# Optimization experiments

Measured on AMD Instinct MI355X. Metric: run time of the kernel, lower is better.

## Reference

```python
import jax, jax.numpy as jnp
import numpy as np

THETA = 10000.0
H, D_NOPE, D_ROPE, D_V = 12, 64, 64, 128
D_MODEL, D_LAT = 768, 128
B, S = 4, 2048


def _rope(x, pos, theta=THETA):
    # x: (B, S, D) with D even; pos: (S,) int. Matches RoPE.forward exactly
    # (interleaved even/odd rotation, freqs over full flattened D).
    D = x.shape[-1]
    inv_freq = 1.0 / theta ** (jnp.arange(0, D, 2, dtype=jnp.float32) / D)
    ang = pos.astype(jnp.float32)[:, None] * inv_freq        # (S, D/2)
    c, s = jnp.cos(ang), jnp.sin(ang)
    xe, xo = x[..., 0::2], x[..., 1::2]
    out = jnp.stack([xe * c - xo * s, xe * s + xo * c], axis=-1)
    return out.reshape(x.shape)


def setup_inputs() -> dict:
    key = jax.random.key(0)
    ks = jax.random.split(key, 12)
    std = 0.02
    inp = {
        'x': jax.random.normal(ks[0], (B, S, D_MODEL), jnp.float32),
        'token_positions': jnp.arange(S, dtype=jnp.int64) if jax.config.jax_enable_x64 else jnp.arange(S, dtype=jnp.int32),
        'W_dkv': jax.random.normal(ks[1], (D_LAT, D_MODEL), jnp.float32) * std,
        'b_dkv': jnp.zeros((D_LAT,), jnp.float32),
        'W_dq': jax.random.normal(ks[2], (D_LAT, D_MODEL), jnp.float32) * std,
        'b_dq': jnp.zeros((D_LAT,), jnp.float32),
        'W_uk_nope': jax.random.normal(ks[3], (H * D_NOPE, D_LAT), jnp.float32) * std,
        'b_uk_nope': jnp.zeros((H * D_NOPE,), jnp.float32),
        'W_uv': jax.random.normal(ks[4], (H * D_V, D_LAT), jnp.float32) * std,
        'b_uv': jnp.zeros((H * D_V,), jnp.float32),
        'W_uq_nope': jax.random.normal(ks[5], (H * D_NOPE, D_LAT), jnp.float32) * std,
        'b_uq_nope': jnp.zeros((H * D_NOPE,), jnp.float32),
        'W_uq_rope': jax.random.normal(ks[6], (H * D_ROPE, D_LAT), jnp.float32) * std,
        'b_uq_rope': jnp.zeros((H * D_ROPE,), jnp.float32),
        'W_uk_rope': jax.random.normal(ks[7], (H * D_ROPE, D_MODEL), jnp.float32) * std,
        'b_uk_rope': jnp.zeros((H * D_ROPE,), jnp.float32),
        'W_o': jax.random.normal(ks[8], (D_MODEL, H * D_V), jnp.float32) * std,
        'b_o': jnp.zeros((D_MODEL,), jnp.float32),
    }
    return inp


def reference(x, token_positions, W_dkv, b_dkv, W_dq, b_dq,
              W_uk_nope, b_uk_nope, W_uv, b_uv, W_uq_nope, b_uq_nope,
              W_uq_rope, b_uq_rope, W_uk_rope, b_uk_rope, W_o, b_o):
    b, s, _ = x.shape
    lin = lambda t, W, bb: t @ W.T + bb
    d_qk = D_NOPE + D_ROPE  # 128

    C_kv = lin(x, W_dkv, b_dkv)               # (B,S,128)
    C_q = lin(x, W_dq, b_dq)                  # (B,S,128)

    q_nope = lin(C_q, W_uq_nope, b_uq_nope)   # (B,S,H*64)
    k_nope = lin(C_kv, W_uk_nope, b_uk_nope)  # (B,S,H*64)
    v = lin(C_kv, W_uv, b_uv)                 # (B,S,H*128)

    q_rope = _rope(lin(C_q, W_uq_rope, b_uq_rope), token_positions)
    k_rope = _rope(lin(x, W_uk_rope, b_uk_rope), token_positions)

    # Faithful to torch: concat flattened nope||rope then view into heads.
    q = jnp.concatenate([q_nope, q_rope], axis=-1).reshape(b, s, H, d_qk).transpose(0, 2, 1, 3)
    k = jnp.concatenate([k_nope, k_rope], axis=-1).reshape(b, s, H, d_qk).transpose(0, 2, 1, 3)
    vh = v.reshape(b, s, H, D_V).transpose(0, 2, 1, 3)

    scale = 1.0 / jnp.sqrt(jnp.asarray(d_qk, x.dtype))
    logits = jnp.einsum('bhqd,bhkd->bhqk', q, k) * scale
    causal = jnp.tril(jnp.ones((s, s), bool))
    logits = jnp.where(causal, logits, jnp.finfo(logits.dtype).min)
    attn = jax.nn.softmax(logits, axis=-1)
    o = jnp.einsum('bhqk,bhkd->bhqd', attn, vh)      # (B,H,S,Dv)
    o = o.transpose(0, 2, 1, 3).reshape(b, s, H * D_V)
    return o @ W_o.T + b_o
```

## Files before the change

### kernel.cpp

```cpp
#include <hip/hip_runtime.h>

typedef __attribute__((ext_vector_type(8))) short short8;
typedef __attribute__((ext_vector_type(4))) short short4v;
typedef __attribute__((ext_vector_type(2))) int int2v;
typedef __attribute__((ext_vector_type(4))) float float4v;

#define MFMA16(a, b, c) __builtin_amdgcn_mfma_f32_16x16x32_bf16((a), (b), (c), 0, 0, 0)

__device__ __forceinline__ short f2bf(float f) {
  unsigned u = __float_as_uint(f);
  u += 0x7fffu + ((u >> 16) & 1u);
  return (short)(u >> 16);
}

__device__ __forceinline__ int cvtpk(float a, float b) {
  int r;
  asm("v_cvt_pk_bf16_f32 %0, %1, %2" : "=v"(r) : "v"(a), "v"(b));
  return r;
}

__device__ __forceinline__ void glds16(const short* g, short* l) {
  __builtin_amdgcn_global_load_lds(
      (const __attribute__((address_space(1))) void*)g,
      (__attribute__((address_space(3))) void*)l, 16, 0, 0);
}

struct CastSeg { const float* src; short* dst; int n4; };
struct CastArgs { CastSeg seg[9]; int start[10]; };

__global__ __launch_bounds__(256) void castk(CastArgs a) {
  int blk = blockIdx.x;
  int si = 0;
#pragma unroll
  for (int i = 1; i < 9; i++) si += (blk >= a.start[i]);
  int i = (blk - a.start[si]) * 256 + threadIdx.x;
  if (i >= a.seg[si].n4) return;
  float4v f = ((const float4v*)a.seg[si].src)[i];
  short4v o;
  o[0] = f2bf(f[0]); o[1] = f2bf(f[1]); o[2] = f2bf(f[2]); o[3] = f2bf(f[3]);
  ((short4v*)a.seg[si].dst)[i] = o;
}

struct GSeg {
  const short* A;
  const short* W;
  const float* bias0;
  const float* bias1;
  void* outp;
  int lda, ldw, bsplit, ropestart, ldo, ocol, K, flags;
};
struct GArgs { GSeg s[3]; int start[4]; };

__global__ __launch_bounds__(256, 2) void gemm_rt(GArgs ga, const int* __restrict__ pos) {
  int bx = blockIdx.x;
  int si = (bx >= ga.start[1]) + (bx >= ga.start[2]);
  const GSeg sg = ga.s[si];
  int tid = threadIdx.x, w = tid >> 6, lane = tid & 63;
  int quad = lane >> 4, l16 = lane & 15;
  int bm = blockIdx.y * 128, bn = (bx - ga.start[si]) * 128;
  int wm = (w & 1) * 64, wn = (w >> 1) * 64;
  int lda = sg.lda, ldw = sg.ldw;

  __shared__ short At[2][128 * 64];
  __shared__ short Bt[2][128 * 64];

  int srow[4], soff[4];
#pragma unroll
  for (int j = 0; j < 4; j++) {
    int r = w * 32 + j * 8 + (lane >> 3);
    srow[j] = r;
    soff[j] = ((lane & 7) ^ (r & 7)) << 3;
  }
  const short* Ag = sg.A + (size_t)bm * lda;
  const short* Wg = sg.W + (size_t)bn * ldw;

  float4v acc[4][4];
  float4v z = {0.f, 0.f, 0.f, 0.f};
#pragma unroll
  for (int mi = 0; mi < 4; mi++)
#pragma unroll
    for (int ni = 0; ni < 4; ni++) acc[mi][ni] = z;

  auto comp = [&](const short* Ab, const short* Bb) {
#pragma unroll
    for (int ks = 0; ks < 2; ks++) {
      short8 af[4], bf[4];
#pragma unroll
      for (int mi = 0; mi < 4; mi++) {
        int row = wm + mi * 16 + l16;
        af[mi] = *(const short8*)&Ab[(row << 6) + ((((ks << 2) + quad) ^ (row & 7)) << 3)];
      }
#pragma unroll
      for (int ni = 0; ni < 4; ni++) {
        int row = wn + ni * 16 + l16;
        bf[ni] = *(const short8*)&Bb[(row << 6) + ((((ks << 2) + quad) ^ (row & 7)) << 3)];
      }
#pragma unroll
      for (int mi = 0; mi < 4; mi++)
#pragma unroll
        for (int ni = 0; ni < 4; ni++)
          acc[mi][ni] = MFMA16(af[mi], bf[ni], acc[mi][ni]);
    }
  };

  int nk = sg.K >> 6;
  if (nk == 2) {
#pragma unroll
    for (int j = 0; j < 4; j++) {
      glds16(Ag + (size_t)srow[j] * lda + soff[j], &At[0][(w * 32 + j * 8) * 64]);
      glds16(Ag + (size_t)srow[j] * lda + 64 + soff[j], &At[1][(w * 32 + j * 8) * 64]);
      glds16(Wg + (size_t)srow[j] * ldw + soff[j], &Bt[0][(w * 32 + j * 8) * 64]);
      glds16(Wg + (size_t)srow[j] * ldw + 64 + soff[j], &Bt[1][(w * 32 + j * 8) * 64]);
    }
    __syncthreads();
    comp(At[0], Bt[0]);
    comp(At[1], Bt[1]);
  } else {
#pragma unroll
    for (int j = 0; j < 4; j++)
      glds16(Ag + (size_t)srow[j] * lda + soff[j], &At[0][(w * 32 + j * 8) * 64]);
#pragma unroll
    for (int j = 0; j < 4; j++)
      glds16(Wg + (size_t)srow[j] * ldw + soff[j], &Bt[0][(w * 32 + j * 8) * 64]);
    for (int it = 0; it < nk; it++) {
      __syncthreads();
      if (it + 1 < nk) {
        int kt = (it + 1) << 6, nb = (it + 1) & 1;
#pragma unroll
        for (int j = 0; j < 4; j++)
          glds16(Ag + (size_t)srow[j] * lda + kt + soff[j],
                 &At[nb][(w * 32 + j * 8) * 64]);
#pragma unroll
        for (int j = 0; j < 4; j++)
          glds16(Wg + (size_t)srow[j] * ldw + kt + soff[j],
                 &Bt[nb][(w * 32 + j * 8) * 64]);
      }
      comp(At[it & 1], Bt[it & 1]);
    }
  }

  bool ropeF = sg.flags & 1, scaleF = sg.flags & 2;
  bool vtF = sg.flags & 4, f32F = sg.flags & 8;
#pragma unroll
  for (int ni = 0; ni < 4; ni++) {
    int col = bn + wn + ni * 16 + l16;
    float bv = (col < sg.bsplit) ? sg.bias0[col] : sg.bias1[col - sg.bsplit];
    float fr = 0.f;
    bool dorope = ropeF && (col >= sg.ropestart);
    if (dorope) {
      int ri = (col - sg.ropestart) & ~1;
      fr = exp2f((float)ri * (-13.287712379549449f / 768.0f));
    }
#pragma unroll
    for (int mi = 0; mi < 4; mi++) {
      int row0 = bm + wm + mi * 16 + quad * 4;
      if (vtF) {
        int bidx = row0 >> 11, s = row0 & 2047;
        short4v ov;
#pragma unroll
        for (int r = 0; r < 4; r++) ov[r] = f2bf(acc[mi][ni][r] + bv);
        *(short4v*)((short*)sg.outp + ((size_t)(bidx * 1536 + col)) * 2048 + s) = ov;
      } else {
#pragma unroll
        for (int r = 0; r < 4; r++) {
          int row = row0 + r;
          float v = acc[mi][ni][r] + bv;
          if (ropeF) {
            float pv = __shfl_xor(v, 1, 64);
            if (dorope) {
              float ang = (float)pos[row & 2047] * fr;
              float sn, cs;
              __sincosf(ang, &sn, &cs);
              v = (col & 1) ? (pv * sn + v * cs) : (v * cs - pv * sn);
            }
          }
          if (scaleF) v *= 0.12751743f;
          if (f32F)
            ((float*)sg.outp)[(size_t)row * sg.ldo + sg.ocol + col] = v;
          else
            ((short*)sg.outp)[(size_t)row * sg.ldo + sg.ocol + col] = f2bf(v);
        }
      }
    }
  }
}

__global__ __launch_bounds__(256, 2) void mla_attn(const short* __restrict__ Q,
                                                   const short* __restrict__ K,
                                                   const short* __restrict__ Vt,
                                                   short* __restrict__ O) {
  const int ld = 1536, SEQ = 2048;
  int tid = threadIdx.x, w = tid >> 6, lane = tid & 63;
  int quad = lane >> 4, l16 = lane & 15;
  int o = (int)blockIdx.x;
  int rank = o / 48;
  int g = o - rank * 48;
  int qt = (15 - rank) * 128;
  int hh = g % 12, b = g / 12;
  int qw = qt + w * 32;

  __shared__ short Kt[2][64 * 128];
  __shared__ short Vl[2][128 * 64];
  __shared__ short Pm[4][32 * 64];
  char* pwB = (char*)Pm[w];

  int kgo[4], vgo[4];
#pragma unroll
  for (int j = 0; j < 4; j++) {
    int rk = (w * 4 + j) * 4 + (lane >> 4);
    kgo[j] = rk * ld + (((lane & 15) ^ (rk & 7)) << 3);
    int rv = (w * 4 + j) * 8 + (lane >> 3);
    vgo[j] = rv * SEQ + (((lane & 7) ^ (rv & 7)) << 3);
  }
  const short* Kg = K + (size_t)b * SEQ * ld + hh * 128;
  const short* Vg = Vt + (size_t)(b * 12 + hh) * 128 * SEQ;

  short8 qf[2][4];
  {
    const short* Qg = Q + (size_t)(b * SEQ + qw + l16) * ld + hh * 128 + quad * 8;
#pragma unroll
    for (int nf = 0; nf < 2; nf++)
#pragma unroll
      for (int ks = 0; ks < 4; ks++)
        qf[nf][ks] = *(const short8*)(Qg + (size_t)nf * 16 * ld + ks * 32);
  }

  int koff[4][4], voff[2][8], pfo[2][2], pwo[2][4];
#pragma unroll
  for (int ks = 0; ks < 4; ks++)
#pragma unroll
    for (int mf = 0; mf < 4; mf++) {
      int row = mf * 16 + l16;
      koff[ks][mf] = row * 256 + ((((ks << 2) + quad) ^ (row & 7)) << 4);
    }
#pragma unroll
  for (int t = 0; t < 2; t++) {
#pragma unroll
    for (int df = 0; df < 8; df++) {
      int vr = df * 16 + l16;
      voff[t][df] = vr * 128 + ((((t << 2) + quad) ^ (vr & 7)) << 4);
    }
#pragma unroll
    for (int mq = 0; mq < 2; mq++)
      pfo[t][mq] = (mq * 16 + l16) * 128 + ((((t << 2) + quad) ^ (l16 & 7)) << 4);
#pragma unroll
    for (int mf = 0; mf < 4; mf++) {
      int p = (mf * 2 + (quad >> 1)) ^ (l16 & 7);
      pwo[t][mf] = (t * 16 + l16) * 128 + (p << 4) + ((quad & 1) << 3);
    }
  }

  float4v z = {0.f, 0.f, 0.f, 0.f};
  float4v oacc[2][8];
#pragma unroll
  for (int mq = 0; mq < 2; mq++)
#pragma unroll
    for (int df = 0; df < 8; df++) oacc[mq][df] = z;
  float l_i[2] = {0.f, 0.f};

#pragma unroll
  for (int j = 0; j < 4; j++) glds16(Kg + kgo[j], &Kt[0][(w * 4 + j) * 512]);
#pragma unroll
  for (int j = 0; j < 4; j++) glds16(Vg + vgo[j], &Vl[0][(w * 4 + j) * 512]);

  int ntiles = (qt >> 6) + 2;

#define ATTN_TILE(IT, NB, NB1)                                                 \
  do {                                                                         \
    int kt = (IT) << 6;                                                        \
    __syncthreads();                                                           \
    if ((IT) + 1 < ntiles) {                                                   \
      const short* kn = Kg + (size_t)(kt + 64) * ld;                           \
      const short* vn = Vg + (kt + 64);                                        \
      _Pragma("unroll") for (int j = 0; j < 4; j++)                            \
          glds16(kn + kgo[j], &Kt[NB1][(w * 4 + j) * 512]);                    \
      _Pragma("unroll") for (int j = 0; j < 4; j++)                            \
          glds16(vn + vgo[j], &Vl[NB1][(w * 4 + j) * 512]);                    \
    }                                                                          \
    if (kt <= qw + 31) {                                                       \
      const char* Kb = (const char*)Kt[NB];                                    \
      const char* Vb = (const char*)Vl[NB];                                    \
      float4v sf[4][2];                                                        \
      __builtin_amdgcn_s_setprio(1);                                           \
      _Pragma("unroll") for (int mf = 0; mf < 4; mf++) {                       \
        short8 a = *(const short8*)(Kb + koff[0][mf]);                         \
        sf[mf][0] = MFMA16(a, qf[0][0], z);                                    \
        sf[mf][1] = MFMA16(a, qf[1][0], z);                                    \
      }                                                                        \
      _Pragma("unroll") for (int ks = 1; ks < 4; ks++) {                       \
        _Pragma("unroll") for (int mf = 0; mf < 4; mf++) {                     \
          short8 a = *(const short8*)(Kb + koff[ks][mf]);                      \
          sf[mf][0] = MFMA16(a, qf[0][ks], sf[mf][0]);                         \
          sf[mf][1] = MFMA16(a, qf[1][ks], sf[mf][1]);                         \
        }                                                                      \
      }                                                                        \
      __builtin_amdgcn_s_setprio(0);                                           \
      if (kt + 63 > qw) {                                                      \
        _Pragma("unroll") for (int mf = 0; mf < 4; mf++) {                     \
          int key = kt + mf * 16 + quad * 4;                                   \
          _Pragma("unroll") for (int nf = 0; nf < 2; nf++) {                   \
            int q = qw + nf * 16 + l16;                                        \
            _Pragma("unroll") for (int r = 0; r < 4; r++)                      \
                if (key + r > q) sf[mf][nf][r] = -3e38f;                       \
          }                                                                    \
        }                                                                      \
      }                                                                        \
      _Pragma("unroll") for (int nf = 0; nf < 2; nf++) {                       \
        float ps = 0.f;                                                        \
        _Pragma("unroll") for (int mf = 0; mf < 4; mf++)                       \
            _Pragma("unroll") for (int r = 0; r < 4; r++) {                    \
          float e = exp2f(sf[mf][nf][r]);                                      \
          sf[mf][nf][r] = e;                                                   \
          ps += e;                                                             \
        }                                                                      \
        l_i[nf] += ps;                                                         \
        _Pragma("unroll") for (int mf = 0; mf < 4; mf++) {                     \
          int2v pk;                                                            \
          pk[0] = cvtpk(sf[mf][nf][0], sf[mf][nf][1]);                         \
          pk[1] = cvtpk(sf[mf][nf][2], sf[mf][nf][3]);                         \
          *(int2v*)(pwB + pwo[nf][mf]) = pk;                                   \
        }                                                                      \
      }                                                                        \
      __builtin_amdgcn_s_setprio(1);                                           \
      _Pragma("unroll") for (int t = 0; t < 2; t++) {                          \
        short8 pf0 = *(const short8*)(pwB + pfo[t][0]);                        \
        short8 pf1 = *(const short8*)(pwB + pfo[t][1]);                        \
        _Pragma("unroll") for (int df = 0; df < 8; df++) {                     \
          short8 vf = *(const short8*)(Vb + voff[t][df]);                      \
          oacc[0][df] = MFMA16(pf0, vf, oacc[0][df]);                          \
          oacc[1][df] = MFMA16(pf1, vf, oacc[1][df]);                          \
        }                                                                      \
      }                                                                        \
      __builtin_amdgcn_s_setprio(0);                                           \
    }                                                                          \
  } while (0)

  for (int it = 0; it < ntiles; it += 2) {
    ATTN_TILE(it, 0, 1);
    ATTN_TILE(it + 1, 1, 0);
  }
#undef ATTN_TILE

  short* Og = O + (size_t)(b * SEQ + qw) * ld + hh * 128;
#pragma unroll
  for (int mq = 0; mq < 2; mq++) {
    float l = l_i[mq];
    l += __shfl_xor(l, 16, 64);
    l += __shfl_xor(l, 32, 64);
    float linv = 1.0f / l;
    float lb[4];
#pragma unroll
    for (int r = 0; r < 4; r++) lb[r] = __shfl(linv, (quad << 2) + r, 64);
#pragma unroll
    for (int df = 0; df < 8; df++)
#pragma unroll
      for (int r = 0; r < 4; r++)
        Og[(size_t)(mq * 16 + (quad << 2) + r) * ld + df * 16 + l16] =
            f2bf(oacc[mq][df][r] * lb[r]);
  }
}

extern "C" void kernel_launch(void* const* d_in, const int* in_sizes, int n_in,
                              void* d_out, int out_size, void* d_ws, size_t ws_size,
                              hipStream_t stream) {
  const int S = 2048, DM = 768, DL = 128, HD = 1536;
  const int M = 4 * S;
  const int BIG = 1 << 28;

  const float* x = (const float*)d_in[0];
  const int* pos = (const int*)d_in[1];
  const float* W_dkv = (const float*)d_in[2];
  const float* b_dkv = (const float*)d_in[3];
  const float* W_dq = (const float*)d_in[4];
  const float* b_dq = (const float*)d_in[5];
  const float* W_uk_nope = (const float*)d_in[6];
  const float* b_uk_nope = (const float*)d_in[7];
  const float* W_uv = (const float*)d_in[8];
  const float* b_uv = (const float*)d_in[9];
  const float* W_uq_nope = (const float*)d_in[10];
  const float* b_uq_nope = (const float*)d_in[11];
  const float* W_uq_rope = (const float*)d_in[12];
  const float* b_uq_rope = (const float*)d_in[13];
  const float* W_uk_rope = (const float*)d_in[14];
  const float* b_uk_rope = (const float*)d_in[15];
  const float* W_o = (const float*)d_in[16];
  const float* b_o = (const float*)d_in[17];

  char* p = (char*)d_ws;
  size_t off = 0;
  auto take = [&](size_t nelem) -> short* {
    short* r = (short*)(p + off);
    off += (nelem * 2 + 255) & ~(size_t)255;
    return r;
  };
  short* xb = take((size_t)M * DM);
  short* Wdq = take(DL * DM);
  short* Wdkv = take(DL * DM);
  short* Wuqnope = take(768 * DL);
  short* Wuqrope = take(768 * DL);
  short* Wuknope = take(768 * DL);
  short* Wuv = take(1536 * DL);
  short* Wukrope = take(768 * DM);
  short* Wo = take(768 * 1536);
  short* Cm = take((size_t)M * 256);
  short* Qm = take((size_t)M * HD);
  short* Km = take((size_t)M * HD);
  short* Vtm = take((size_t)M * HD);
  short* Om = take((size_t)M * HD);
  if (off > ws_size) return;

  CastArgs ca;
  const float* srcs[9] = {x, W_dq, W_dkv, W_uq_nope, W_uq_rope, W_uk_nope, W_uv, W_uk_rope, W_o};
  short* dsts[9] = {xb, Wdq, Wdkv, Wuqnope, Wuqrope, Wuknope, Wuv, Wukrope, Wo};
  int ns[9] = {M * DM, DL * DM, DL * DM, 768 * DL, 768 * DL, 768 * DL, 1536 * DL, 768 * DM, 768 * 1536};
  ca.start[0] = 0;
  for (int i = 0; i < 9; i++) {
    ca.seg[i].src = srcs[i];
    ca.seg[i].dst = dsts[i];
    ca.seg[i].n4 = ns[i] / 4;
    ca.start[i + 1] = ca.start[i] + (ca.seg[i].n4 + 255) / 256;
  }
  castk<<<dim3(ca.start[9]), dim3(256), 0, stream>>>(ca);

  GArgs g1;
  g1.s[0].A = xb;   g1.s[0].W = Wdq;      g1.s[0].bias0 = b_dq;      g1.s[0].bias1 = b_dkv;
  g1.s[0].outp = Cm; g1.s[0].lda = DM; g1.s[0].ldw = DM; g1.s[0].bsplit = 128;
  g1.s[0].ropestart = 0; g1.s[0].ldo = 256; g1.s[0].ocol = 0; g1.s[0].K = DM; g1.s[0].flags = 0;
  g1.s[1].A = xb;   g1.s[1].W = Wukrope;  g1.s[1].bias0 = b_uk_rope; g1.s[1].bias1 = b_uk_rope;
  g1.s[1].outp = Km; g1.s[1].lda = DM; g1.s[1].ldw = DM; g1.s[1].bsplit = BIG;
  g1.s[1].ropestart = 0; g1.s[1].ldo = HD; g1.s[1].ocol = 768; g1.s[1].K = DM; g1.s[1].flags = 1;
  g1.s[2] = g1.s[1];
  g1.start[0] = 0; g1.start[1] = 2; g1.start[2] = 8; g1.start[3] = 8;
  gemm_rt<<<dim3(8, M / 128), dim3(256), 0, stream>>>(g1, pos);

  GArgs g2;
  g2.s[0].A = Cm;   g2.s[0].W = Wuqnope;  g2.s[0].bias0 = b_uq_nope; g2.s[0].bias1 = b_uq_rope;
  g2.s[0].outp = Qm; g2.s[0].lda = 256; g2.s[0].ldw = DL; g2.s[0].bsplit = 768;
  g2.s[0].ropestart = 768; g2.s[0].ldo = HD; g2.s[0].ocol = 0; g2.s[0].K = DL; g2.s[0].flags = 1 | 2;
  g2.s[1].A = Cm + 128; g2.s[1].W = Wuknope; g2.s[1].bias0 = b_uk_nope; g2.s[1].bias1 = b_uk_nope;
  g2.s[1].outp = Km; g2.s[1].lda = 256; g2.s[1].ldw = DL; g2.s[1].bsplit = BIG;
  g2.s[1].ropestart = 0; g2.s[1].ldo = HD; g2.s[1].ocol = 0; g2.s[1].K = DL; g2.s[1].flags = 0;
  g2.s[2].A = Cm + 128; g2.s[2].W = Wuv;   g2.s[2].bias0 = b_uv;      g2.s[2].bias1 = b_uv;
  g2.s[2].outp = Vtm; g2.s[2].lda = 256; g2.s[2].ldw = DL; g2.s[2].bsplit = BIG;
  g2.s[2].ropestart = 0; g2.s[2].ldo = 0; g2.s[2].ocol = 0; g2.s[2].K = DL; g2.s[2].flags = 4;
  g2.start[0] = 0; g2.start[1] = 12; g2.start[2] = 18; g2.start[3] = 30;
  gemm_rt<<<dim3(30, M / 128), dim3(256), 0, stream>>>(g2, pos);

  mla_attn<<<dim3(768), dim3(256), 0, stream>>>(Qm, Km, Vtm, Om);

  GArgs g3;
  g3.s[0].A = Om;   g3.s[0].W = Wo;       g3.s[0].bias0 = b_o;       g3.s[0].bias1 = b_o;
  g3.s[0].outp = d_out; g3.s[0].lda = HD; g3.s[0].ldw = HD; g3.s[0].bsplit = BIG;
  g3.s[0].ropestart = 0; g3.s[0].ldo = 768; g3.s[0].ocol = 0; g3.s[0].K = HD; g3.s[0].flags = 8;
  g3.s[1] = g3.s[0];
  g3.s[2] = g3.s[0];
  g3.start[0] = 0; g3.start[1] = 6; g3.start[2] = 6; g3.start[3] = 6;
  gemm_rt<<<dim3(6, M / 128), dim3(256), 0, stream>>>(g3, pos);
}
```

Before: 311.0 us.

## Reuse A tile across paired N tiles and stage V-transpose stores via LDS

For the K=128 up-projection GEMMs, a block now loads its A tile once and computes two 128-wide N tiles in sequence (pairF flag). The second W tile is staged while the first epilogue runs, so A global traffic and the block count drop. The V-transposed output is now staged through shared memory with a rotated layout and written as coalesced 16-byte rows instead of scattered 8-byte stores. The grid is transposed so M tiles lie along x, which changes block scheduling order. The cost is fewer blocks (less parallelism) and extra barriers inside each block.

```diff
diff --git a/kernel.cpp b/kernel.cpp
--- a/kernel.cpp
+++ b/kernel.cpp
@@ -52,12 +52,15 @@
 struct GArgs { GSeg s[3]; int start[4]; };
 
 __global__ __launch_bounds__(256, 2) void gemm_rt(GArgs ga, const int* __restrict__ pos) {
-  int bx = blockIdx.x;
-  int si = (bx >= ga.start[1]) + (bx >= ga.start[2]);
+  int by = blockIdx.y;
+  int si = (by >= ga.start[1]) + (by >= ga.start[2]);
   const GSeg sg = ga.s[si];
   int tid = threadIdx.x, w = tid >> 6, lane = tid & 63;
   int quad = lane >> 4, l16 = lane & 15;
-  int bm = blockIdx.y * 128, bn = (bx - ga.start[si]) * 128;
+  bool ropeF = sg.flags & 1, scaleF = sg.flags & 2;
+  bool vtF = sg.flags & 4, f32F = sg.flags & 8, pairF = sg.flags & 16;
+  int bm = blockIdx.x * 128;
+  int bn = (by - ga.start[si]) * (pairF ? 256 : 128);
   int wm = (w & 1) * 64, wn = (w >> 1) * 64;
   int lda = sg.lda, ldw = sg.ldw;
 
@@ -103,64 +106,50 @@
     }
   };
 
-  int nk = sg.K >> 6;
-  if (nk == 2) {
-#pragma unroll
-    for (int j = 0; j < 4; j++) {
-      glds16(Ag + (size_t)srow[j] * lda + soff[j], &At[0][(w * 32 + j * 8) * 64]);
-      glds16(Ag + (size_t)srow[j] * lda + 64 + soff[j], &At[1][(w * 32 + j * 8) * 64]);
-      glds16(Wg + (size_t)srow[j] * ldw + soff[j], &Bt[0][(w * 32 + j * 8) * 64]);
-      glds16(Wg + (size_t)srow[j] * ldw + 64 + soff[j], &Bt[1][(w * 32 + j * 8) * 64]);
-    }
-    __syncthreads();
-    comp(At[0], Bt[0]);
-    comp(At[1], Bt[1]);
-  } else {
-#pragma unroll
-    for (int j = 0; j < 4; j++)
-      glds16(Ag + (size_t)srow[j] * lda + soff[j], &At[0][(w * 32 + j * 8) * 64]);
-#pragma unroll
-    for (int j = 0; j < 4; j++)
-      glds16(Wg + (size_t)srow[j] * ldw + soff[j], &Bt[0][(w * 32 + j * 8) * 64]);
-    for (int it = 0; it < nk; it++) {
+  auto epi = [&](int bnX) {
+    if (vtF) {
       __syncthreads();
-      if (it + 1 < nk) {
-        int kt = (it + 1) << 6, nb = (it + 1) & 1;
-#pragma unroll
-        for (int j = 0; j < 4; j++)
-          glds16(Ag + (size_t)srow[j] * lda + kt + soff[j],
-                 &At[nb][(w * 32 + j * 8) * 64]);
-#pragma unroll
-        for (int j = 0; j < 4; j++)
-          glds16(Wg + (size_t)srow[j] * ldw + kt + soff[j],
-                 &Bt[nb][(w * 32 + j * 8) * 64]);
-      }
-      comp(At[it & 1], Bt[it & 1]);
-    }
-  }
-
-  bool ropeF = sg.flags & 1, scaleF = sg.flags & 2;
-  bool vtF = sg.flags & 4, f32F = sg.flags & 8;
-#pragma unroll
-  for (int ni = 0; ni < 4; ni++) {
-    int col = bn + wn + ni * 16 + l16;
-    float bv = (col < sg.bsplit) ? sg.bias0[col] : sg.bias1[col - sg.bsplit];
-    float fr = 0.f;
-    bool dorope = ropeF && (col >= sg.ropestart);
-    if (dorope) {
-      int ri = (col - sg.ropestart) & ~1;
-      fr = exp2f((float)ri * (-13.287712379549449f / 768.0f));
-    }
-#pragma unroll
-    for (int mi = 0; mi < 4; mi++) {
-      int row0 = bm + wm + mi * 16 + quad * 4;
-      if (vtF) {
-        int bidx = row0 >> 11, s = row0 & 2047;
-        short4v ov;
-#pragma unroll
-        for (int r = 0; r < 4; r++) ov[r] = f2bf(acc[mi][ni][r] + bv);
-        *(short4v*)((short*)sg.outp + ((size_t)(bidx * 1536 + col)) * 2048 + s) = ov;
-      } else {
+      short* T = &At[0][0];
+#pragma unroll
+      for (int ni = 0; ni < 4; ni++) {
+        int col = wn + ni * 16 + l16;
+        float bv = sg.bias0[bnX + col];
+#pragma unroll
+        for (int mi = 0; mi < 4; mi++) {
+          int row0 = wm + mi * 16 + quad * 4;
+          int rr = (row0 + ((col & 15) << 3)) & 127;
+          short4v ov;
+#pragma unroll
+          for (int r = 0; r < 4; r++) ov[r] = f2bf(acc[mi][ni][r] + bv);
+          *(short4v*)&T[col * 128 + rr] = ov;
+        }
+      }
+      __syncthreads();
+      int bidx = bm >> 11, s0 = bm & 2047;
+      int sc = tid & 15;
+#pragma unroll
+      for (int cc = 0; cc < 8; cc++) {
+        int c = cc * 16 + (tid >> 4);
+        int rr = ((sc + (c & 15)) << 3) & 127;
+        short8 v = *(const short8*)&T[c * 128 + rr];
+        *(short8*)((short*)sg.outp + ((size_t)(bidx * 1536 + bnX + c)) * 2048 +
+                   s0 + (sc << 3)) = v;
+      }
+      return;
+    }
+#pragma unroll
+    for (int ni = 0; ni < 4; ni++) {
+      int col = bnX + wn + ni * 16 + l16;
+      float bv = (col < sg.bsplit) ? sg.bias0[col] : sg.bias1[col - sg.bsplit];
+      float fr = 0.f;
+      bool dorope = ropeF && (col >= sg.ropestart);
+      if (dorope) {
+        int ri = (col - sg.ropestart) & ~1;
+        fr = exp2f((float)ri * (-13.287712379549449f / 768.0f));
+      }
+#pragma unroll
+      for (int mi = 0; mi < 4; mi++) {
+        int row0 = bm + wm + mi * 16 + quad * 4;
 #pragma unroll
         for (int r = 0; r < 4; r++) {
           int row = row0 + r;
@@ -182,6 +171,64 @@
         }
       }
     }
+  };
+
+  int nk = sg.K >> 6;
+  if (nk == 2) {
+    auto stageB = [&](const short* Wg2) {
+#pragma unroll
+      for (int j = 0; j < 4; j++) {
+        glds16(Wg2 + (size_t)srow[j] * ldw + soff[j], &Bt[0][(w * 32 + j * 8) * 64]);
+        glds16(Wg2 + (size_t)srow[j] * ldw + 64 + soff[j], &Bt[1][(w * 32 + j * 8) * 64]);
+      }
+    };
+#pragma unroll
+    for (int j = 0; j < 4; j++) {
+      glds16(Ag + (size_t)srow[j] * lda + soff[j], &At[0][(w * 32 + j * 8) * 64]);
+      glds16(Ag + (size_t)srow[j] * lda + 64 + soff[j], &At[1][(w * 32 + j * 8) * 64]);
+    }
+    stageB(Wg);
+    __syncthreads();
+    comp(At[0], Bt[0]);
+    comp(At[1], Bt[1]);
+    if (pairF) {
+      __syncthreads();
+      stageB(Wg + (size_t)128 * ldw);
+      epi(bn);
+#pragma unroll
+      for (int mi = 0; mi < 4; mi++)
+#pragma unroll
+        for (int ni = 0; ni < 4; ni++) acc[mi][ni] = z;
+      __syncthreads();
+      comp(At[0], Bt[0]);
+      comp(At[1], Bt[1]);
+      epi(bn + 128);
+    } else {
+      epi(bn);
+    }
+  } else {
+#pragma unroll
+    for (int j = 0; j < 4; j++)
+      glds16(Ag + (size_t)srow[j] * lda + soff[j], &At[0][(w * 32 + j * 8) * 64]);
+#pragma unroll
+    for (int j = 0; j < 4; j++)
+      glds16(Wg + (size_t)srow[j] * ldw + soff[j], &Bt[0][(w * 32 + j * 8) * 64]);
+    for (int it = 0; it < nk; it++) {
+      __syncthreads();
+      if (it + 1 < nk) {
+        int kt = (it + 1) << 6, nb = (it + 1) & 1;
+#pragma unroll
+        for (int j = 0; j < 4; j++)
+          glds16(Ag + (size_t)srow[j] * lda + kt + soff[j],
+                 &At[nb][(w * 32 + j * 8) * 64]);
+#pragma unroll
+        for (int j = 0; j < 4; j++)
+          glds16(Wg + (size_t)srow[j] * ldw + kt + soff[j],
+                 &Bt[nb][(w * 32 + j * 8) * 64]);
+      }
+      comp(At[it & 1], Bt[it & 1]);
+    }
+    epi(bn);
   }
 }
 
@@ -431,20 +478,23 @@
   g1.s[1].ropestart = 0; g1.s[1].ldo = HD; g1.s[1].ocol = 768; g1.s[1].K = DM; g1.s[1].flags = 1;
   g1.s[2] = g1.s[1];
   g1.start[0] = 0; g1.start[1] = 2; g1.start[2] = 8; g1.start[3] = 8;
-  gemm_rt<<<dim3(8, M / 128), dim3(256), 0, stream>>>(g1, pos);
+  gemm_rt<<<dim3(M / 128, 8), dim3(256), 0, stream>>>(g1, pos);
 
   GArgs g2;
   g2.s[0].A = Cm;   g2.s[0].W = Wuqnope;  g2.s[0].bias0 = b_uq_nope; g2.s[0].bias1 = b_uq_rope;
   g2.s[0].outp = Qm; g2.s[0].lda = 256; g2.s[0].ldw = DL; g2.s[0].bsplit = 768;
-  g2.s[0].ropestart = 768; g2.s[0].ldo = HD; g2.s[0].ocol = 0; g2.s[0].K = DL; g2.s[0].flags = 1 | 2;
+  g2.s[0].ropestart = 768; g2.s[0].ldo = HD; g2.s[0].ocol = 0; g2.s[0].K = DL;
+  g2.s[0].flags = 1 | 2 | 16;
   g2.s[1].A = Cm + 128; g2.s[1].W = Wuknope; g2.s[1].bias0 = b_uk_nope; g2.s[1].bias1 = b_uk_nope;
   g2.s[1].outp = Km; g2.s[1].lda = 256; g2.s[1].ldw = DL; g2.s[1].bsplit = BIG;
-  g2.s[1].ropestart = 0; g2.s[1].ldo = HD; g2.s[1].ocol = 0; g2.s[1].K = DL; g2.s[1].flags = 0;
+  g2.s[1].ropestart = 0; g2.s[1].ldo = HD; g2.s[1].ocol = 0; g2.s[1].K = DL;
+  g2.s[1].flags = 16;
   g2.s[2].A = Cm + 128; g2.s[2].W = Wuv;   g2.s[2].bias0 = b_uv;      g2.s[2].bias1 = b_uv;
   g2.s[2].outp = Vtm; g2.s[2].lda = 256; g2.s[2].ldw = DL; g2.s[2].bsplit = BIG;
-  g2.s[2].ropestart = 0; g2.s[2].ldo = 0; g2.s[2].ocol = 0; g2.s[2].K = DL; g2.s[2].flags = 4;
-  g2.start[0] = 0; g2.start[1] = 12; g2.start[2] = 18; g2.start[3] = 30;
-  gemm_rt<<<dim3(30, M / 128), dim3(256), 0, stream>>>(g2, pos);
+  g2.s[2].ropestart = 0; g2.s[2].ldo = 0; g2.s[2].ocol = 0; g2.s[2].K = DL;
+  g2.s[2].flags = 4;
+  g2.start[0] = 0; g2.start[1] = 6; g2.start[2] = 9; g2.start[3] = 21;
+  gemm_rt<<<dim3(M / 128, 21), dim3(256), 0, stream>>>(g2, pos);
 
   mla_attn<<<dim3(768), dim3(256), 0, stream>>>(Qm, Km, Vtm, Om);
 
@@ -455,5 +505,5 @@
   g3.s[1] = g3.s[0];
   g3.s[2] = g3.s[0];
   g3.start[0] = 0; g3.start[1] = 6; g3.start[2] = 6; g3.start[3] = 6;
-  gemm_rt<<<dim3(6, M / 128), dim3(256), 0, stream>>>(g3, pos);
-}
+  gemm_rt<<<dim3(M / 128, 6), dim3(256), 0, stream>>>(g3, pos);
+}
```

After: 304.3 us. 2.2% less time.
